# Kernel tuning notes

Hardware: AMD Instinct MI355X
Metric: run time of the kernel (lower is better)

The kernel has to match this reference:

```python
import jax, jax.numpy as jnp
import numpy as np

N_HEADS = 16
HEAD = 64
HID = 1024
WIN = 256
LN_EPS = 1e-5


def _ln(x, g, b):
    m = jnp.mean(x, axis=-1, keepdims=True)
    v = jnp.mean((x - m) ** 2, axis=-1, keepdims=True)
    return (x - m) * jax.lax.rsqrt(v + LN_EPS) * g + b


def _window_shift(x):
    return jnp.concatenate([jnp.zeros_like(x[:, :WIN]), x[:, :-WIN]], axis=1)


def _additive_attn(x, vec, mask_add):
    B, S, _ = x.shape
    # per-head logits: (x * vec) summed within each head, scaled
    attn = (x * vec).reshape(B, S, N_HEADS, HEAD).sum(-1) / (HEAD ** 0.5)
    attn = jnp.exp(attn + mask_add)[..., None]          # [B,S,H,1]
    xh = x.reshape(B, S, N_HEADS, HEAD)
    s = jnp.cumsum(attn * xh, axis=1)
    s = s - _window_shift(s)                             # windowed cumsum of attn*x
    z = jnp.cumsum(attn, axis=1)
    z = z - _window_shift(z)                             # windowed cumsum of attn
    return (s / z).reshape(B, S, HID)


def setup_inputs():
    key = jax.random.key(0)
    ks = jax.random.split(key, 7)
    B, S = 4, 4096
    w = lambda k: (jax.random.normal(k, (HID, HID)) * 0.02).astype(jnp.float32)
    return {
        "hidden_states": jax.random.normal(ks[0], (B, S, HID), dtype=jnp.float32),
        "attention_mask": jnp.ones((B, S), dtype=jnp.float32),
        "Wq": w(ks[1]), "Wk": w(ks[2]), "Wv": w(ks[3]), "Wp": w(ks[4]),
        "query_attn": (jax.random.normal(ks[5], (HID,)) * 0.02).astype(jnp.float32),
        "key_attn": (jax.random.normal(ks[6], (HID,)) * 0.02).astype(jnp.float32),
        "ln1_g": jnp.ones((HID,), jnp.float32), "ln1_b": jnp.zeros((HID,), jnp.float32),
        "ln2_g": jnp.ones((HID,), jnp.float32), "ln2_b": jnp.zeros((HID,), jnp.float32),
    }


def reference(hidden_states, attention_mask, Wq, Wk, Wv, Wp, query_attn, key_attn,
              ln1_g, ln1_b, ln2_g, ln2_b):
    h = _ln(hidden_states, ln1_g, ln1_b)
    query = h @ Wq.T
    keys = h @ Wk.T
    values = h @ Wv.T
    mask_add = ((1.0 - attention_mask) * -10000.0)[:, :, None]  # [B,S,1]
    pooled_q = _additive_attn(query, query_attn, mask_add)
    pooled_q = pooled_q @ Wp.T                                  # (dropout is identity in eval)
    residual = h + pooled_q * keys
    mixed = _ln(residual, ln2_g, ln2_b)
    pooled_k = _additive_attn(mixed, key_attn, mask_add)
    return residual + pooled_k * values
```

## Files before the change

kernel.cpp:

```cpp
#include <hip/hip_runtime.h>
#include <hip/hip_bf16.h>

#define HID 1024
#define NH 16
#define HEAD 64
#define WIN 256
#define SEQ 4096
#define BATCH 4
#define NROWS (BATCH * SEQ)
#define LN_EPS 1e-5f

typedef unsigned short u16;
typedef __bf16 bf16x8 __attribute__((ext_vector_type(8)));
typedef float f32x4 __attribute__((ext_vector_type(4)));

static __device__ inline float bfu(u16 u) {
    union { unsigned int i; float f; } x;
    x.i = ((unsigned int)u) << 16;
    return x.f;
}

static __device__ inline u16 f2bf(float f) {
    union { float f; unsigned int i; } x;
    x.f = f;
    unsigned int lsb = (x.i >> 16) & 1u;
    x.i += 0x7fffu + lsb;
    return (u16)(x.i >> 16);
}

__global__ __launch_bounds__(256) void convert_weights(
    const float* __restrict__ wq, const float* __restrict__ wk,
    const float* __restrict__ wv, const float* __restrict__ wp,
    u16* __restrict__ o)
{
    int i = blockIdx.x * 256 + threadIdx.x;
    const int n = 1024 * 1024;
    if (i < n) {
        o[i]         = f2bf(wq[i]);
        o[n + i]     = f2bf(wk[i]);
        o[2 * n + i] = f2bf(wv[i]);
        o[3 * n + i] = f2bf(wp[i]);
    }
}

__global__ __launch_bounds__(256) void ln1_kernel(
    const float* __restrict__ x, const float* __restrict__ g,
    const float* __restrict__ b, u16* __restrict__ out)
{
    int row = blockIdx.x;
    int t = threadIdx.x;
    float4 v = ((const float4*)(x + (size_t)row * HID))[t];
    float s  = v.x + v.y + v.z + v.w;
    float ss = v.x * v.x + v.y * v.y + v.z * v.z + v.w * v.w;
    __shared__ float red[8];
    #pragma unroll
    for (int off = 32; off; off >>= 1) { s += __shfl_down(s, off); ss += __shfl_down(ss, off); }
    int wave = t >> 6, lane = t & 63;
    if (lane == 0) { red[wave] = s; red[4 + wave] = ss; }
    __syncthreads();
    float S  = red[0] + red[1] + red[2] + red[3];
    float SS = red[4] + red[5] + red[6] + red[7];
    float mean = S * (1.f / HID);
    float var  = SS * (1.f / HID) - mean * mean;
    float inv  = rsqrtf(var + LN_EPS);
    float4 gv = ((const float4*)g)[t];
    float4 bv = ((const float4*)b)[t];
    ushort4 o;
    o.x = f2bf((v.x - mean) * inv * gv.x + bv.x);
    o.y = f2bf((v.y - mean) * inv * gv.y + bv.y);
    o.z = f2bf((v.z - mean) * inv * gv.z + bv.z);
    o.w = f2bf((v.w - mean) * inv * gv.w + bv.w);
    ((ushort4*)(out + (size_t)row * HID))[t] = o;
}

__global__ __launch_bounds__(256) void gemm_bt(
    const u16* __restrict__ A, const u16* __restrict__ W,
    u16* __restrict__ C, int M, int N, int K, int ldc)
{
    __shared__ __align__(16) u16 sA[2][128 * 32];
    __shared__ __align__(16) u16 sB[2][128 * 32];

    int t = threadIdx.x;
    int bm = blockIdx.x, bn = blockIdx.y;
    int wave = t >> 6, lane = t & 63;
    int wr = wave >> 1, wc = wave & 1;

    f32x4 acc[4][4];
    #pragma unroll
    for (int m = 0; m < 4; ++m)
        #pragma unroll
        for (int n = 0; n < 4; ++n) {
            f32x4 z = {0.f, 0.f, 0.f, 0.f};
            acc[m][n] = z;
        }

    const int nk = K >> 5;

    auto stage = [&](int buf, int kt) {
        int k0 = kt << 5;
        #pragma unroll
        for (int i = 0; i < 2; ++i) {
            int ch = i * 256 + t;
            int row = ch >> 2, kc = (ch & 3) << 3;
            const u16* ga = A + (size_t)(bm * 128 + row) * K + k0 + kc;
            __builtin_amdgcn_global_load_lds(
                (const __attribute__((address_space(1))) void*)ga,
                (__attribute__((address_space(3))) void*)&sA[buf][ch * 8], 16, 0, 0);
            const u16* gb = W + (size_t)(bn * 128 + row) * K + k0 + kc;
            __builtin_amdgcn_global_load_lds(
                (const __attribute__((address_space(1))) void*)gb,
                (__attribute__((address_space(3))) void*)&sB[buf][ch * 8], 16, 0, 0);
        }
    };

    stage(0, 0);
    int cur = 0;
    for (int kt = 0; kt < nk; ++kt) {
        asm volatile("s_waitcnt vmcnt(0)" ::: "memory");
        __syncthreads();
        if (kt + 1 < nk) stage(cur ^ 1, kt + 1);

        int arow = wr * 64 + (lane & 15);
        int brow = wc * 64 + (lane & 15);
        int kg = (lane >> 4) << 3;
        bf16x8 af[4], bfv[4];
        #pragma unroll
        for (int m = 0; m < 4; ++m)
            af[m] = *(const bf16x8*)&sA[cur][(arow + m * 16) * 32 + kg];
        #pragma unroll
        for (int n = 0; n < 4; ++n)
            bfv[n] = *(const bf16x8*)&sB[cur][(brow + n * 16) * 32 + kg];
        #pragma unroll
        for (int m = 0; m < 4; ++m)
            #pragma unroll
            for (int n = 0; n < 4; ++n)
                acc[m][n] = __builtin_amdgcn_mfma_f32_16x16x32_bf16(af[m], bfv[n], acc[m][n], 0, 0, 0);

        cur ^= 1;
    }

    #pragma unroll
    for (int m = 0; m < 4; ++m) {
        int row0 = bm * 128 + wr * 64 + m * 16 + ((lane >> 4) << 2);
        #pragma unroll
        for (int n = 0; n < 4; ++n) {
            int col = bn * 128 + wc * 64 + n * 16 + (lane & 15);
            #pragma unroll
            for (int r = 0; r < 4; ++r)
                C[(size_t)(row0 + r) * ldc + col] = f2bf(acc[m][n][r]);
        }
    }
}

__global__ __launch_bounds__(256) void logits_kernel(
    const u16* __restrict__ x, int xstride,
    const float* __restrict__ vec, const float* __restrict__ mask,
    float* __restrict__ aw)
{
    int h = blockIdx.y, b = blockIdx.z;
    int s = blockIdx.x * 256 + threadIdx.x;
    __shared__ float vl[HEAD];
    if (threadIdx.x < HEAD) vl[threadIdx.x] = vec[h * HEAD + threadIdx.x];
    __syncthreads();
    const uint4* xr = (const uint4*)(x + ((size_t)(b * SEQ + s)) * xstride + h * HEAD);
    float dot = 0.f;
    #pragma unroll
    for (int i = 0; i < 8; ++i) {
        uint4 v = xr[i];
        const u16* p = (const u16*)&v;
        #pragma unroll
        for (int j = 0; j < 8; ++j) dot += bfu(p[j]) * vl[i * 8 + j];
    }
    float ma = (1.0f - mask[b * SEQ + s]) * -10000.0f;
    aw[((size_t)b * NH + h) * SEQ + s] = expf(dot * 0.125f + ma);
}

__global__ __launch_bounds__(256) void attn_win(
    const u16* __restrict__ x, int xstride,
    const float* __restrict__ aw_g,
    u16* __restrict__ out)
{
    int c = blockIdx.x, h = blockIdx.y, b = blockIdx.z;
    __shared__ float awl[2][WIN];
    __shared__ float sts[2][4][HEAD];
    __shared__ float stz[2][4];

    int t = threadIdx.x, wave = t >> 6, lane = t & 63;
    bool havePrev = (c > 0);

    const float* awb = aw_g + ((size_t)b * NH + h) * SEQ;
    for (int i = t; i < 2 * WIN; i += 256) {
        int cc = i >> 8, j = i & (WIN - 1);
        float v = 0.f;
        if (cc == 1) v = awb[c * WIN + j];
        else if (havePrev) v = awb[(c - 1) * WIN + j];
        awl[cc][j] = v;
    }
    __syncthreads();

    const u16* xb = x + (size_t)b * SEQ * xstride + h * HEAD + lane;
    int jp0 = (havePrev ? (c - 1) : c) * WIN;
    int jc0 = c * WIN;
    int j0 = wave << 6;

    float s0 = 0.f, s1 = 0.f, z0 = 0.f, z1 = 0.f;
    #pragma unroll 8
    for (int jj = 0; jj < 64; ++jj) {
        int j = j0 + jj;
        float ap = awl[0][j], ac = awl[1][j];
        float xp = bfu(xb[(size_t)(jp0 + j) * xstride]);
        float xc = bfu(xb[(size_t)(jc0 + j) * xstride]);
        s0 += ap * xp; z0 += ap;
        s1 += ac * xc; z1 += ac;
    }
    sts[0][wave][lane] = s0;
    sts[1][wave][lane] = s1;
    if (lane == 0) { stz[0][wave] = z0; stz[1][wave] = z1; }
    __syncthreads();

    float cs0 = 0.f, cs1 = 0.f, cz0 = 0.f, cz1 = 0.f, tots = 0.f, totz = 0.f;
    #pragma unroll
    for (int w2 = 0; w2 < 4; ++w2) {
        float sp = sts[0][w2][lane], zp = stz[0][w2];
        tots += sp; totz += zp;
        if (w2 < wave) {
            cs0 += sp; cz0 += zp;
            cs1 += sts[1][w2][lane]; cz1 += stz[1][w2];
        }
    }

    float rp = cs0, rc = cs1, rzp = cz0, rzc = cz1;
    size_t obase = ((size_t)b * SEQ + c * WIN) * HID + h * HEAD + lane;
    #pragma unroll 8
    for (int jj = 0; jj < 64; ++jj) {
        int j = j0 + jj;
        float ap = awl[0][j], ac = awl[1][j];
        float xp = bfu(xb[(size_t)(jp0 + j) * xstride]);
        float xc = bfu(xb[(size_t)(jc0 + j) * xstride]);
        rp += ap * xp; rzp += ap;
        rc += ac * xc; rzc += ac;
        float swin = rc + tots - rp;
        float zwin = rzc + totz - rzp;
        out[obase + (size_t)j * HID] = f2bf(swin / zwin);
    }
}

__global__ __launch_bounds__(256) void resid_ln2(
    const u16* h, const u16* __restrict__ qkv,
    const float* __restrict__ g, const float* __restrict__ b,
    const float* __restrict__ ka, const float* __restrict__ mask,
    float* __restrict__ residual, u16* mixed, float* __restrict__ aw2)
{
    int row = blockIdx.x;
    int t = threadIdx.x;
    ushort4 h4 = ((const ushort4*)(h + (size_t)row * HID))[t];
    ushort4 p4 = ((const ushort4*)(qkv + (size_t)row * 3072))[t];
    ushort4 k4 = ((const ushort4*)(qkv + (size_t)row * 3072 + 1024))[t];
    float r0 = bfu(h4.x) + bfu(p4.x) * bfu(k4.x);
    float r1 = bfu(h4.y) + bfu(p4.y) * bfu(k4.y);
    float r2 = bfu(h4.z) + bfu(p4.z) * bfu(k4.z);
    float r3 = bfu(h4.w) + bfu(p4.w) * bfu(k4.w);
    ((float4*)(residual + (size_t)row * HID))[t] = make_float4(r0, r1, r2, r3);

    float s  = r0 + r1 + r2 + r3;
    float ss = r0 * r0 + r1 * r1 + r2 * r2 + r3 * r3;
    __shared__ float red[8];
    #pragma unroll
    for (int off = 32; off; off >>= 1) { s += __shfl_down(s, off); ss += __shfl_down(ss, off); }
    int wave = t >> 6, lane = t & 63;
    if (lane == 0) { red[wave] = s; red[4 + wave] = ss; }
    __syncthreads();
    float S  = red[0] + red[1] + red[2] + red[3];
    float SS = red[4] + red[5] + red[6] + red[7];
    float mean = S * (1.f / HID);
    float var  = SS * (1.f / HID) - mean * mean;
    float inv  = rsqrtf(var + LN_EPS);
    float4 gv = ((const float4*)g)[t];
    float4 bv = ((const float4*)b)[t];
    float n0 = (r0 - mean) * inv * gv.x + bv.x;
    float n1 = (r1 - mean) * inv * gv.y + bv.y;
    float n2 = (r2 - mean) * inv * gv.z + bv.z;
    float n3 = (r3 - mean) * inv * gv.w + bv.w;
    ushort4 o;
    o.x = f2bf(n0); o.y = f2bf(n1); o.z = f2bf(n2); o.w = f2bf(n3);
    ((ushort4*)(mixed + (size_t)row * HID))[t] = o;

    float4 kv = ((const float4*)ka)[t];
    float partial = n0 * kv.x + n1 * kv.y + n2 * kv.z + n3 * kv.w;
    partial += __shfl_xor(partial, 1);
    partial += __shfl_xor(partial, 2);
    partial += __shfl_xor(partial, 4);
    partial += __shfl_xor(partial, 8);
    if ((t & 15) == 0) {
        int hh = t >> 4;
        int bb = row >> 12, sl = row & (SEQ - 1);
        float ma = (1.0f - mask[row]) * -10000.0f;
        aw2[((size_t)bb * NH + hh) * SEQ + sl] = expf(partial * 0.125f + ma);
    }
}

__global__ __launch_bounds__(256) void final_kernel(
    float* out, const u16* __restrict__ pk,
    const u16* __restrict__ qkv, int total4)
{
    for (int i = blockIdx.x * blockDim.x + threadIdx.x; i < total4; i += gridDim.x * blockDim.x) {
        int e = i * 4;
        int r = e >> 10;
        int cc = e & 1023;
        float4 rv = ((const float4*)out)[i];
        ushort4 pv = ((const ushort4*)pk)[i];
        ushort4 vv = *(const ushort4*)(qkv + (size_t)r * 3072 + 2048 + cc);
        float4 o;
        o.x = rv.x + bfu(pv.x) * bfu(vv.x);
        o.y = rv.y + bfu(pv.y) * bfu(vv.y);
        o.z = rv.z + bfu(pv.z) * bfu(vv.z);
        o.w = rv.w + bfu(pv.w) * bfu(vv.w);
        ((float4*)out)[i] = o;
    }
}

extern "C" void kernel_launch(void* const* d_in, const int* in_sizes, int n_in,
                              void* d_out, int out_size, void* d_ws, size_t ws_size,
                              hipStream_t stream)
{
    const float* hidden = (const float*)d_in[0];
    const float* mask   = (const float*)d_in[1];
    const float* Wq     = (const float*)d_in[2];
    const float* Wk     = (const float*)d_in[3];
    const float* Wv     = (const float*)d_in[4];
    const float* Wp     = (const float*)d_in[5];
    const float* qa     = (const float*)d_in[6];
    const float* ka     = (const float*)d_in[7];
    const float* g1     = (const float*)d_in[8];
    const float* b1     = (const float*)d_in[9];
    const float* g2     = (const float*)d_in[10];
    const float* b2     = (const float*)d_in[11];
    float* out = (float*)d_out;

    char* ws = (char*)d_ws;
    u16* wbf = (u16*)ws;       ws += (size_t)4 * 1024 * 1024 * 2;
    u16* hbf = (u16*)ws;       ws += (size_t)NROWS * HID * 2;
    u16* qkv = (u16*)ws;       ws += (size_t)NROWS * 3072 * 2;
    u16* pooled = (u16*)ws;    ws += (size_t)NROWS * HID * 2;
    float* aw1 = (float*)ws;   ws += (size_t)BATCH * NH * SEQ * 4;
    float* aw2 = (float*)ws;

    convert_weights<<<4096, 256, 0, stream>>>(Wq, Wk, Wv, Wp, wbf);
    ln1_kernel<<<NROWS, 256, 0, stream>>>(hidden, g1, b1, hbf);
    gemm_bt<<<dim3(128, 24), 256, 0, stream>>>(hbf, wbf, qkv, NROWS, 3072, HID, 3072);
    logits_kernel<<<dim3(SEQ / 256, NH, BATCH), 256, 0, stream>>>(qkv, 3072, qa, mask, aw1);
    attn_win<<<dim3(SEQ / WIN, NH, BATCH), 256, 0, stream>>>(qkv, 3072, aw1, pooled);
    gemm_bt<<<dim3(128, 8), 256, 0, stream>>>(pooled, wbf + (size_t)3 * 1024 * 1024, qkv,
                                              NROWS, HID, HID, 3072);
    resid_ln2<<<NROWS, 256, 0, stream>>>(hbf, qkv, g2, b2, ka, mask, out, hbf, aw2);
    attn_win<<<dim3(SEQ / WIN, NH, BATCH), 256, 0, stream>>>(hbf, HID, aw2, pooled);
    final_kernel<<<2048, 256, 0, stream>>>(out, pooled, qkv, NROWS * HID / 4);
}
```

Before: 333.4 us.

## Replace GEMM with 256x256 swizzled pipelined kernel and fuse final residual into attention

Swaps the 128x128 bf16 GEMM for a 512-thread 256x256-tile kernel. It uses a 64-wide K step, XOR-swizzled LDS layout, phased double-buffered global-to-LDS prefetch with fine-grained waitcnt, setprio around the MFMA bursts, and an XCD-aware block remap. Separately, the second windowed-attention pass now writes residual + pooled*values directly into the fp32 output, which removes the final elementwise kernel and its pooled round trip. The larger tile cuts reload traffic per output but raises register and LDS pressure, and the fused path does read-modify-write on the output with strided access.

```diff
diff --git a/kernel.cpp b/kernel.cpp
--- a/kernel.cpp
+++ b/kernel.cpp
@@ -73,81 +73,116 @@
     ((ushort4*)(out + (size_t)row * HID))[t] = o;
 }
 
-__global__ __launch_bounds__(256) void gemm_bt(
+#define GLDS(gp, lp) __builtin_amdgcn_global_load_lds( \
+    (const __attribute__((address_space(1))) void*)(gp), \
+    (__attribute__((address_space(3))) void*)(lp), 16, 0, 0)
+
+#define PHASE(P, STAGE_CODE, WAIT_CODE)                                        \
+  {                                                                            \
+    bf16x8 aF[2][2], bF[4][2];                                                 \
+    _Pragma("unroll") for (int e = 0; e < 2; ++e)                              \
+      _Pragma("unroll") for (int kh = 0; kh < 2; ++kh)                         \
+        aF[e][kh] = *(const bf16x8*)&rA[(P) * 4096 +                           \
+            (wr * 32 + e * 16 + (lane & 15)) * 64 + ((c0 ^ (kh << 6)) >> 1)];  \
+    _Pragma("unroll") for (int n = 0; n < 4; ++n)                              \
+      _Pragma("unroll") for (int kh = 0; kh < 2; ++kh)                         \
+        bF[n][kh] = *(const bf16x8*)&rB[wc * 4096 +                            \
+            (n * 16 + (lane & 15)) * 64 + ((c0 ^ (kh << 6)) >> 1)];            \
+    STAGE_CODE                                                                 \
+    WAIT_CODE                                                                  \
+    __builtin_amdgcn_s_barrier();                                              \
+    __builtin_amdgcn_sched_barrier(0);                                         \
+    __builtin_amdgcn_s_setprio(1);                                             \
+    _Pragma("unroll") for (int e = 0; e < 2; ++e)                              \
+      _Pragma("unroll") for (int n = 0; n < 4; ++n)                            \
+        _Pragma("unroll") for (int kh = 0; kh < 2; ++kh)                       \
+          acc[2 * (P) + e][n] = __builtin_amdgcn_mfma_f32_16x16x32_bf16(       \
+              aF[e][kh], bF[n][kh], acc[2 * (P) + e][n], 0, 0, 0);             \
+    __builtin_amdgcn_s_setprio(0);                                             \
+    __builtin_amdgcn_s_barrier();                                              \
+    __builtin_amdgcn_sched_barrier(0);                                         \
+  }
+
+__global__ __launch_bounds__(512, 2) void gemm256(
     const u16* __restrict__ A, const u16* __restrict__ W,
-    u16* __restrict__ C, int M, int N, int K, int ldc)
-{
-    __shared__ __align__(16) u16 sA[2][128 * 32];
-    __shared__ __align__(16) u16 sB[2][128 * 32];
-
-    int t = threadIdx.x;
-    int bm = blockIdx.x, bn = blockIdx.y;
-    int wave = t >> 6, lane = t & 63;
-    int wr = wave >> 1, wc = wave & 1;
-
-    f32x4 acc[4][4];
-    #pragma unroll
-    for (int m = 0; m < 4; ++m)
+    u16* __restrict__ C, int K, int ldc, int nbm)
+{
+    __shared__ __align__(16) u16 sA[2][256 * 64];
+    __shared__ __align__(16) u16 sB[2][256 * 64];
+
+    const int tid = threadIdx.x;
+    const int cpx = gridDim.x >> 3;
+    const int wg = (blockIdx.x & 7) * cpx + (blockIdx.x >> 3);
+    const int bm = wg % nbm, bn = wg / nbm;
+
+    const int wave = tid >> 6, lane = tid & 63;
+    const int wr = wave >> 2, wc = wave & 3;
+
+    const int rp = tid >> 3;
+    const int colE = (((tid & 7) * 16) ^ ((rp & 7) << 4)) >> 1;
+    const u16* gA = A + (size_t)(bm * 256 + (rp < 32 ? rp : rp + 96)) * K + colE;
+    const u16* gB = W + (size_t)(bn * 256 + rp) * K + colE;
+
+    const int c0 = ((lane >> 4) * 16) ^ ((lane & 7) << 4);
+
+    f32x4 acc[8][4];
+    #pragma unroll
+    for (int m = 0; m < 8; ++m)
         #pragma unroll
         for (int n = 0; n < 4; ++n) {
             f32x4 z = {0.f, 0.f, 0.f, 0.f};
             acc[m][n] = z;
         }
 
-    const int nk = K >> 5;
-
-    auto stage = [&](int buf, int kt) {
-        int k0 = kt << 5;
-        #pragma unroll
-        for (int i = 0; i < 2; ++i) {
-            int ch = i * 256 + t;
-            int row = ch >> 2, kc = (ch & 3) << 3;
-            const u16* ga = A + (size_t)(bm * 128 + row) * K + k0 + kc;
-            __builtin_amdgcn_global_load_lds(
-                (const __attribute__((address_space(1))) void*)ga,
-                (__attribute__((address_space(3))) void*)&sA[buf][ch * 8], 16, 0, 0);
-            const u16* gb = W + (size_t)(bn * 128 + row) * K + k0 + kc;
-            __builtin_amdgcn_global_load_lds(
-                (const __attribute__((address_space(1))) void*)gb,
-                (__attribute__((address_space(3))) void*)&sB[buf][ch * 8], 16, 0, 0);
-        }
-    };
-
-    stage(0, 0);
-    int cur = 0;
+    const int nk = K >> 6;
+
+    #pragma unroll
+    for (int w = 0; w < 4; ++w) GLDS(gB + (size_t)w * 64 * K, &sB[0][w * 4096 + tid * 8]);
+    #pragma unroll
+    for (int p = 0; p < 4; ++p) GLDS(gA + (size_t)p * 32 * K, &sA[0][p * 4096 + tid * 8]);
+    asm volatile("s_waitcnt vmcnt(3)" ::: "memory");
+    __builtin_amdgcn_s_barrier();
+    __builtin_amdgcn_sched_barrier(0);
+
     for (int kt = 0; kt < nk; ++kt) {
-        asm volatile("s_waitcnt vmcnt(0)" ::: "memory");
-        __syncthreads();
-        if (kt + 1 < nk) stage(cur ^ 1, kt + 1);
-
-        int arow = wr * 64 + (lane & 15);
-        int brow = wc * 64 + (lane & 15);
-        int kg = (lane >> 4) << 3;
-        bf16x8 af[4], bfv[4];
-        #pragma unroll
-        for (int m = 0; m < 4; ++m)
-            af[m] = *(const bf16x8*)&sA[cur][(arow + m * 16) * 32 + kg];
-        #pragma unroll
-        for (int n = 0; n < 4; ++n)
-            bfv[n] = *(const bf16x8*)&sB[cur][(brow + n * 16) * 32 + kg];
-        #pragma unroll
-        for (int m = 0; m < 4; ++m)
-            #pragma unroll
-            for (int n = 0; n < 4; ++n)
-                acc[m][n] = __builtin_amdgcn_mfma_f32_16x16x32_bf16(af[m], bfv[n], acc[m][n], 0, 0, 0);
-
-        cur ^= 1;
-    }
-
-    #pragma unroll
-    for (int m = 0; m < 4; ++m) {
-        int row0 = bm * 128 + wr * 64 + m * 16 + ((lane >> 4) << 2);
+        const int b = kt & 1;
+        const u16* rA = sA[b];
+        const u16* rB = sB[b];
+        u16* dA = sA[b ^ 1];
+        u16* dB = sB[b ^ 1];
+        const bool pf = (kt + 1 < nk);
+        const size_t ko = (size_t)(kt + 1) * 64;
+
+        PHASE(0,
+            { if (pf) { GLDS(gB + ko,                    &dB[0 * 4096 + tid * 8]);
+                        GLDS(gB + (size_t)1 * 64 * K + ko, &dB[1 * 4096 + tid * 8]); } },
+            { if (pf) asm volatile("s_waitcnt vmcnt(4)" ::: "memory");
+              else    asm volatile("s_waitcnt vmcnt(2)" ::: "memory"); })
+        PHASE(1,
+            { if (pf) { GLDS(gB + (size_t)2 * 64 * K + ko, &dB[2 * 4096 + tid * 8]);
+                        GLDS(gB + (size_t)3 * 64 * K + ko, &dB[3 * 4096 + tid * 8]); } },
+            { if (pf) asm volatile("s_waitcnt vmcnt(5)" ::: "memory");
+              else    asm volatile("s_waitcnt vmcnt(1)" ::: "memory"); })
+        PHASE(2,
+            { if (pf) { GLDS(gA + ko,                    &dA[0 * 4096 + tid * 8]);
+                        GLDS(gA + (size_t)1 * 32 * K + ko, &dA[1 * 4096 + tid * 8]); } },
+            { if (pf) asm volatile("s_waitcnt vmcnt(6)" ::: "memory");
+              else    asm volatile("s_waitcnt vmcnt(0)" ::: "memory"); })
+        PHASE(3,
+            { if (pf) { GLDS(gA + (size_t)2 * 32 * K + ko, &dA[2 * 4096 + tid * 8]);
+                        GLDS(gA + (size_t)3 * 32 * K + ko, &dA[3 * 4096 + tid * 8]); } },
+            { if (pf) asm volatile("s_waitcnt vmcnt(3)" ::: "memory"); })
+    }
+
+    #pragma unroll
+    for (int mf = 0; mf < 8; ++mf) {
+        int row0 = bm * 256 + wr * 128 + mf * 16 + ((lane >> 4) << 2);
         #pragma unroll
         for (int n = 0; n < 4; ++n) {
-            int col = bn * 128 + wc * 64 + n * 16 + (lane & 15);
+            int col = bn * 256 + wc * 64 + n * 16 + (lane & 15);
             #pragma unroll
             for (int r = 0; r < 4; ++r)
-                C[(size_t)(row0 + r) * ldc + col] = f2bf(acc[m][n][r]);
+                C[(size_t)(row0 + r) * ldc + col] = f2bf(acc[mf][n][r]);
         }
     }
 }
@@ -178,7 +213,10 @@
 __global__ __launch_bounds__(256) void attn_win(
     const u16* __restrict__ x, int xstride,
     const float* __restrict__ aw_g,
-    u16* __restrict__ out)
+    u16* __restrict__ out_bf,
+    const u16* __restrict__ vsrc,
+    float* __restrict__ outF,
+    int fused)
 {
     int c = blockIdx.x, h = blockIdx.y, b = blockIdx.z;
     __shared__ float awl[2][WIN];
@@ -231,7 +269,8 @@
 
     float rp = cs0, rc = cs1, rzp = cz0, rzc = cz1;
     size_t obase = ((size_t)b * SEQ + c * WIN) * HID + h * HEAD + lane;
-    #pragma unroll 8
+    size_t vbase = ((size_t)b * SEQ + c * WIN) * 3072 + 2048 + h * HEAD + lane;
+    #pragma unroll 4
     for (int jj = 0; jj < 64; ++jj) {
         int j = j0 + jj;
         float ap = awl[0][j], ac = awl[1][j];
@@ -239,9 +278,13 @@
         float xc = bfu(xb[(size_t)(jc0 + j) * xstride]);
         rp += ap * xp; rzp += ap;
         rc += ac * xc; rzc += ac;
-        float swin = rc + tots - rp;
-        float zwin = rzc + totz - rzp;
-        out[obase + (size_t)j * HID] = f2bf(swin / zwin);
+        float wv = (rc + tots - rp) / (rzc + totz - rzp);
+        if (fused) {
+            size_t oi = obase + (size_t)j * HID;
+            outF[oi] = outF[oi] + wv * bfu(vsrc[vbase + (size_t)j * 3072]);
+        } else {
+            out_bf[obase + (size_t)j * HID] = f2bf(wv);
+        }
     }
 }
 
@@ -299,26 +342,6 @@
     }
 }
 
-__global__ __launch_bounds__(256) void final_kernel(
-    float* out, const u16* __restrict__ pk,
-    const u16* __restrict__ qkv, int total4)
-{
-    for (int i = blockIdx.x * blockDim.x + threadIdx.x; i < total4; i += gridDim.x * blockDim.x) {
-        int e = i * 4;
-        int r = e >> 10;
-        int cc = e & 1023;
-        float4 rv = ((const float4*)out)[i];
-        ushort4 pv = ((const ushort4*)pk)[i];
-        ushort4 vv = *(const ushort4*)(qkv + (size_t)r * 3072 + 2048 + cc);
-        float4 o;
-        o.x = rv.x + bfu(pv.x) * bfu(vv.x);
-        o.y = rv.y + bfu(pv.y) * bfu(vv.y);
-        o.z = rv.z + bfu(pv.z) * bfu(vv.z);
-        o.w = rv.w + bfu(pv.w) * bfu(vv.w);
-        ((float4*)out)[i] = o;
-    }
-}
-
 extern "C" void kernel_launch(void* const* d_in, const int* in_sizes, int n_in,
                               void* d_out, int out_size, void* d_ws, size_t ws_size,
                               hipStream_t stream)
@@ -347,12 +370,12 @@
 
     convert_weights<<<4096, 256, 0, stream>>>(Wq, Wk, Wv, Wp, wbf);
     ln1_kernel<<<NROWS, 256, 0, stream>>>(hidden, g1, b1, hbf);
-    gemm_bt<<<dim3(128, 24), 256, 0, stream>>>(hbf, wbf, qkv, NROWS, 3072, HID, 3072);
+    gemm256<<<768, 512, 0, stream>>>(hbf, wbf, qkv, HID, 3072, 64);
     logits_kernel<<<dim3(SEQ / 256, NH, BATCH), 256, 0, stream>>>(qkv, 3072, qa, mask, aw1);
-    attn_win<<<dim3(SEQ / WIN, NH, BATCH), 256, 0, stream>>>(qkv, 3072, aw1, pooled);
-    gemm_bt<<<dim3(128, 8), 256, 0, stream>>>(pooled, wbf + (size_t)3 * 1024 * 1024, qkv,
-                                              NROWS, HID, HID, 3072);
+    attn_win<<<dim3(SEQ / WIN, NH, BATCH), 256, 0, stream>>>(qkv, 3072, aw1, pooled,
+                                                             (const u16*)nullptr, (float*)nullptr, 0);
+    gemm256<<<256, 512, 0, stream>>>(pooled, wbf + (size_t)3 * 1024 * 1024, qkv, HID, 3072, 64);
     resid_ln2<<<NROWS, 256, 0, stream>>>(hbf, qkv, g2, b2, ka, mask, out, hbf, aw2);
-    attn_win<<<dim3(SEQ / WIN, NH, BATCH), 256, 0, stream>>>(hbf, HID, aw2, pooled);
-    final_kernel<<<2048, 256, 0, stream>>>(out, pooled, qkv, NROWS * HID / 4);
-}
+    attn_win<<<dim3(SEQ / WIN, NH, BATCH), 256, 0, stream>>>(hbf, HID, aw2, pooled,
+                                                             qkv, out, 1);
+}
```

After: 349.5 us. 1.05x slower.
